# Kernel tuning notes

Hardware: AMD Instinct MI355X
Metric: run time of the kernel (lower is better)

Reference implementation:

```python
import jax, jax.numpy as jnp
import numpy as np

B, T, C = 2, 2048, 1024
NH, HD = 16, 64  # n_head, head_dim (qk == vo)


def setup_inputs() -> dict:
    key = jax.random.key(0)
    ks = jax.random.split(key, 5)
    scale = 1.0 / np.sqrt(C)
    return {
        "x": jax.random.normal(ks[0], (B, T, C), dtype=jnp.float32),
        "Wq": jax.random.normal(ks[1], (C, C), dtype=jnp.float32) * scale,
        "Wk": jax.random.normal(ks[2], (C, C), dtype=jnp.float32) * scale,
        "Wv": jax.random.normal(ks[3], (C, C), dtype=jnp.float32) * scale,
        "Wo": jax.random.normal(ks[4], (C, C), dtype=jnp.float32) * scale,
    }


def reference(x, Wq, Wk, Wv, Wo):
    # torch Linear: y = x @ W.T (weights stored [out, in])
    q = (x @ Wq.T).reshape(B, T, NH, HD).transpose(0, 2, 1, 3)  # [B,H,T,D]
    k = (x @ Wk.T).reshape(B, T, NH, HD).transpose(0, 2, 1, 3)
    v = (x @ Wv.T).reshape(B, T, NH, HD).transpose(0, 2, 1, 3)
    att = jnp.einsum("bhqd,bhkd->bhqk", q, k) * (1.0 / np.sqrt(HD))
    causal = jnp.tril(jnp.ones((T, T), dtype=bool))
    att = jnp.where(causal[None, None], att, -jnp.inf)
    att = jax.nn.softmax(att, axis=-1)
    y = jnp.einsum("bhqk,bhkd->bhqd", att, v)  # [B,H,T,D]
    y = y.transpose(0, 2, 1, 3).reshape(B, T, NH * HD)
    return y @ Wo.T  # dropout p=0 -> identity
```

## Files before the change

### kernel.cpp

```cpp
#include <hip/hip_runtime.h>
#include <hip/hip_bf16.h>
#include <cstdint>
#include <cstddef>
#include <cmath>

#define B_  2
#define T_  2048
#define C_  1024
#define NH_ 16
#define HD_ 64

typedef __bf16 bf16;
typedef bf16  bf16x8 __attribute__((ext_vector_type(8)));
typedef bf16  bf16x4 __attribute__((ext_vector_type(4)));
typedef float f32x4  __attribute__((ext_vector_type(4)));
typedef float f32x16 __attribute__((ext_vector_type(16)));

#define MFMA16(a, b, c) __builtin_amdgcn_mfma_f32_16x16x32_bf16((a), (b), (c), 0, 0, 0)
#define MFMA32(a, b, c) __builtin_amdgcn_mfma_f32_32x32x16_bf16((a), (b), (c), 0, 0, 0)

__device__ __forceinline__ void gld_lds16(const bf16* g, bf16* lds_base_uniform) {
    __builtin_amdgcn_global_load_lds(
        (const __attribute__((address_space(1))) uint32_t*)g,
        (__attribute__((address_space(3))) uint32_t*)lds_base_uniform,
        16, 0, 0);
}

__global__ __launch_bounds__(256) void cast_all(const float* __restrict__ x,
                                                const float* __restrict__ Wq,
                                                const float* __restrict__ Wk,
                                                const float* __restrict__ Wv,
                                                const float* __restrict__ Wo,
                                                bf16* __restrict__ xb,
                                                bf16* __restrict__ Wqk,
                                                bf16* __restrict__ Wvb,
                                                bf16* __restrict__ Wob) {
    const int bid = blockIdx.x;
    if (bid < 4096) {
        const int i = bid * 256 + threadIdx.x;
        float4 v = ((const float4*)x)[i];
        ((bf16x4*)xb)[i] = bf16x4{ (bf16)v.x, (bf16)v.y, (bf16)v.z, (bf16)v.w };
    } else {
        const float C1 = 0.1803368801111f;
        const int i = (bid - 4096) * 256 + threadIdx.x;
        const int nw4 = C_ * C_ / 4;
        float4 q = ((const float4*)Wq)[i];
        float4 k = ((const float4*)Wk)[i];
        float4 v = ((const float4*)Wv)[i];
        float4 o = ((const float4*)Wo)[i];
        ((bf16x4*)Wqk)[i]       = bf16x4{ (bf16)(q.x * C1), (bf16)(q.y * C1),
                                          (bf16)(q.z * C1), (bf16)(q.w * C1) };
        ((bf16x4*)Wqk)[nw4 + i] = bf16x4{ (bf16)k.x, (bf16)k.y, (bf16)k.z, (bf16)k.w };
        ((bf16x4*)Wvb)[i]       = bf16x4{ (bf16)v.x, (bf16)v.y, (bf16)v.z, (bf16)v.w };
        ((bf16x4*)Wob)[i]       = bf16x4{ (bf16)o.x, (bf16)o.y, (bf16)o.z, (bf16)o.w };
    }
}

__device__ __forceinline__ void gemm_tile(bf16* As, bf16* Bs,
                                          const bf16* __restrict__ A,
                                          const bf16* __restrict__ W,
                                          bf16* __restrict__ Y,
                                          int N, int K, int m0, int n0) {
    const int tid  = threadIdx.x;
    const int lane = tid & 63;
    const int w    = tid >> 6;
    const int ml   = lane & 15;
    const int quad = lane >> 4;
    const int wm   = (w >> 1) * 64;
    const int wn   = (w & 1) * 64;
    const int sr   = lane >> 2;
    const int sc   = lane & 3;

    f32x4 acc[4][4] = {};

    for (int k0 = 0; k0 < K; k0 += 32) {
        __syncthreads();
#pragma unroll
        for (int ei = 0; ei < 2; ++ei) {
            const int e = w * 2 + ei;
            gld_lds16(A + (size_t)(m0 + e * 16 + sr) * K + k0 + sc * 8, &As[e * 512]);
            gld_lds16(W + (size_t)(n0 + e * 16 + sr) * K + k0 + sc * 8, &Bs[e * 512]);
        }
        __builtin_amdgcn_s_waitcnt(0);
        __syncthreads();

        bf16x8 af[4], bfr[4];
#pragma unroll
        for (int t = 0; t < 4; ++t) {
            af[t]  = *(const bf16x8*)&As[(wm + t * 16 + ml) * 32 + quad * 8];
            bfr[t] = *(const bf16x8*)&Bs[(wn + t * 16 + ml) * 32 + quad * 8];
        }
#pragma unroll
        for (int mt = 0; mt < 4; ++mt)
#pragma unroll
            for (int nt = 0; nt < 4; ++nt)
                acc[mt][nt] = MFMA16(af[mt], bfr[nt], acc[mt][nt]);
    }

#pragma unroll
    for (int mt = 0; mt < 4; ++mt)
#pragma unroll
        for (int nt = 0; nt < 4; ++nt)
#pragma unroll
            for (int r = 0; r < 4; ++r) {
                const int row = m0 + wm + mt * 16 + quad * 4 + r;
                const int col = n0 + wn + nt * 16 + ml;
                Y[(size_t)row * N + col] = (bf16)acc[mt][nt][r];
            }
}

__global__ __launch_bounds__(256) void proj_fused(const bf16* __restrict__ xb,
                                                  const bf16* __restrict__ Wqk,
                                                  const bf16* __restrict__ Wvb,
                                                  bf16* __restrict__ QKb,
                                                  bf16* __restrict__ VtT) {
    __shared__ __align__(16) bf16 As[128 * 32];
    __shared__ __align__(16) bf16 Bs[128 * 32];
    const int bid = blockIdx.x;
    if (bid < 512) {
        gemm_tile(As, Bs, xb, Wqk, QKb, 2048, 1024, (bid >> 4) * 128, (bid & 15) * 128);
    } else {
        const int b2 = bid - 512;
        gemm_tile(As, Bs, Wvb, xb, VtT, 4096, 1024, (b2 >> 5) * 128, (b2 & 31) * 128);
    }
}

__global__ __launch_bounds__(256) void gemm_wo(const bf16* __restrict__ A,
                                               const bf16* __restrict__ W,
                                               float* __restrict__ Y) {
    __shared__ __align__(16) bf16 As[64 * 32];
    __shared__ __align__(16) bf16 Bs[128 * 32];
    const int tid  = threadIdx.x;
    const int lane = tid & 63;
    const int w    = tid >> 6;
    const int ml   = lane & 15;
    const int quad = lane >> 4;
    const int wm   = (w >> 1) * 32;
    const int wn   = (w & 1) * 64;
    const int m0   = blockIdx.y * 64;
    const int n0   = blockIdx.x * 128;
    const int sr   = lane >> 2;
    const int sc   = lane & 3;

    f32x4 acc[2][4] = {};

    for (int k0 = 0; k0 < 1024; k0 += 32) {
        __syncthreads();
        gld_lds16(A + (size_t)(m0 + w * 16 + sr) * 1024 + k0 + sc * 8, &As[w * 512]);
#pragma unroll
        for (int ei = 0; ei < 2; ++ei) {
            const int e = w * 2 + ei;
            gld_lds16(W + (size_t)(n0 + e * 16 + sr) * 1024 + k0 + sc * 8, &Bs[e * 512]);
        }
        __builtin_amdgcn_s_waitcnt(0);
        __syncthreads();

        bf16x8 af[2], bfr[4];
#pragma unroll
        for (int t = 0; t < 2; ++t)
            af[t] = *(const bf16x8*)&As[(wm + t * 16 + ml) * 32 + quad * 8];
#pragma unroll
        for (int t = 0; t < 4; ++t)
            bfr[t] = *(const bf16x8*)&Bs[(wn + t * 16 + ml) * 32 + quad * 8];
#pragma unroll
        for (int mt = 0; mt < 2; ++mt)
#pragma unroll
            for (int nt = 0; nt < 4; ++nt)
                acc[mt][nt] = MFMA16(af[mt], bfr[nt], acc[mt][nt]);
    }

#pragma unroll
    for (int mt = 0; mt < 2; ++mt)
#pragma unroll
        for (int nt = 0; nt < 4; ++nt)
#pragma unroll
            for (int r = 0; r < 4; ++r) {
                const int row = m0 + wm + mt * 16 + quad * 4 + r;
                const int col = n0 + wn + nt * 16 + ml;
                Y[(size_t)row * 1024 + col] = acc[mt][nt][r];
            }
}

__global__ __launch_bounds__(256, 3) void attn_mfma(const bf16* __restrict__ QKb,
                                                    const bf16* __restrict__ VtT,
                                                    bf16* __restrict__ Pbuf,
                                                    float* __restrict__ Lbuf) {
    const int bid = blockIdx.x;
    const int hb  = bid & 31;
    const int s   = 39 - (bid >> 5);
    int it, chunk;
    if (s < 4)       { it = s;                  chunk = 0; }
    else if (s < 12) { it = 4 + ((s - 4) >> 1); chunk = (s - 4) & 1; }
    else if (s < 24) { it = 8 + (s - 12) / 3;   chunk = (s - 12) % 3; }
    else             { it = 12 + ((s - 24) >> 2); chunk = (s - 24) & 3; }
    const int h = hb >> 1, b = hb & 1;

    const int tid  = threadIdx.x;
    const int lane = tid & 63;
    const int w    = tid >> 6;
    const int keyl = lane & 31;
    const int hi   = lane >> 5;

    __shared__ __align__(16) bf16 Ks[2][4096];
    __shared__ __align__(16) bf16 Vs[2][4096];
    __shared__ __align__(16) bf16 Ps[4][2048];

    const bf16* Qbase = QKb + (size_t)b * T_ * 2048 + (size_t)h * HD_;
    const bf16* Kbase = Qbase + 1024;
    const bf16* Vbase = VtT + (size_t)h * HD_ * 4096 + (size_t)b * T_;

    const int qrow = it * 128 + w * 32 + keyl;
    bf16x8 qf[4];
#pragma unroll
    for (int dc = 0; dc < 4; ++dc)
        qf[dc] = *(const bf16x8*)(Qbase + (size_t)qrow * 2048 + dc * 16 + hi * 8);

    f32x16 o_acc[2] = {};
    f32x16 l_acc = {};
    bf16x8 onesf;
#pragma unroll
    for (int j = 0; j < 8; ++j) onesf[j] = (bf16)1.0f;

    bf16* ps = &Ps[w][0];
    uint16_t* ps16 = (uint16_t*)ps;

    const int ktbase  = chunk * 8;
    const int nrounds = min(8, 2 * it + 2 - ktbase);

    auto stageKV = [&](int ktg, int buf) {
        const int k0 = ktg * 64;
#pragma unroll
        for (int ei = 0; ei < 2; ++ei) {
            const int e  = w * 2 + ei;
            const int rr = e * 8 + (lane >> 3);
            const int g  = (lane & 7) ^ (lane >> 3);
            gld_lds16(Kbase + (size_t)(k0 + rr) * 2048 + g * 8, &Ks[buf][e * 512]);
            gld_lds16(Vbase + (size_t)rr * 4096 + k0 + g * 8, &Vs[buf][e * 512]);
        }
    };

    auto phase1 = [&](int cur, int ktg) {
        const int k0 = ktg * 64;
        const bool domask = (k0 + 63) > (it * 128 + w * 32);
#pragma unroll
        for (int kh = 0; kh < 2; ++kh) {
            f32x16 sacc = {};
#pragma unroll
            for (int dc = 0; dc < 4; ++dc) {
                bf16x8 kf = *(const bf16x8*)&Ks[cur][(kh * 32 + keyl) * 64 +
                                                     ((((dc << 1) | hi)) ^ (keyl & 7)) * 8];
                sacc = MFMA32(qf[dc], kf, sacc);
            }
            const int kg = k0 + kh * 32 + keyl;
#pragma unroll
            for (int r = 0; r < 16; ++r) {
                float arg = sacc[r];
                const int qloc = (r & 3) + 8 * (r >> 2) + 4 * hi;
                if (domask) {
                    const int qg = it * 128 + w * 32 + qloc;
                    if (kg > qg) arg = -1e30f;
                }
                const float p = __builtin_amdgcn_exp2f(arg);
                ps16[qloc * 64 + (((kh * 4 + (keyl >> 3)) ^ (qloc & 7)) << 3) + (keyl & 7)] =
                    (uint16_t)(__builtin_bit_cast(uint32_t, p) >> 16);
            }
        }
    };

    auto phase2 = [&](int cur) {
        bf16x8 pa[4];
#pragma unroll
        for (int kc = 0; kc < 4; ++kc) {
            pa[kc] = *(const bf16x8*)&ps[keyl * 64 + (((kc << 1) | hi) ^ (keyl & 7)) * 8];
            l_acc = MFMA32(pa[kc], onesf, l_acc);
        }
#pragma unroll
        for (int dh = 0; dh < 2; ++dh)
#pragma unroll
            for (int kc = 0; kc < 4; ++kc) {
                bf16x8 vf = *(const bf16x8*)&Vs[cur][(dh * 32 + keyl) * 64 +
                                                     (((kc << 1) | hi) ^ (keyl & 7)) * 8];
                o_acc[dh] = MFMA32(pa[kc], vf, o_acc[dh]);
            }
    };

    stageKV(ktbase, 0);
    asm volatile("s_waitcnt vmcnt(0)" ::: "memory");
    asm volatile("s_barrier" ::: "memory");

    for (int j = 0; j < nrounds; ++j) {
        const int cur = j & 1;
        const int ktg = ktbase + j;
        if (j + 1 < nrounds) stageKV(ktg + 1, cur ^ 1);
        phase1(cur, ktg);
        phase2(cur);
        if (j + 1 < nrounds) {
            asm volatile("s_waitcnt vmcnt(0)" ::: "memory");
            asm volatile("s_barrier" ::: "memory");
        }
    }

    const int slotIdx = hb * 40 + s;
    bf16* pb = Pbuf + (size_t)slotIdx * 8192;
#pragma unroll
    for (int dh = 0; dh < 2; ++dh)
#pragma unroll
        for (int r = 0; r < 16; ++r) {
            const int qloc = w * 32 + (r & 3) + 8 * (r >> 2) + 4 * hi;
            pb[qloc * 64 + dh * 32 + keyl] = (bf16)o_acc[dh][r];
        }
    if (keyl == 0) {
#pragma unroll
        for (int r = 0; r < 16; ++r) {
            const int qloc = w * 32 + (r & 3) + 8 * (r >> 2) + 4 * hi;
            Lbuf[slotIdx * 128 + qloc] = l_acc[r];
        }
    }
}

__global__ __launch_bounds__(256) void attn_merge(const bf16* __restrict__ Pbuf,
                                                  const float* __restrict__ Lbuf,
                                                  bf16* __restrict__ Ab) {
    const int gid = blockIdx.x;
    const int it  = gid >> 5;
    const int hb  = gid & 31;
    const int h = hb >> 1, b = hb & 1;
    int s0;
    if (it < 4)       s0 = it;
    else if (it < 8)  s0 = 4 + (it - 4) * 2;
    else if (it < 12) s0 = 12 + (it - 8) * 3;
    else              s0 = 24 + (it - 12) * 4;
    const int nch = (2 * it + 9) >> 3;

    const int tid = threadIdx.x;
    const int row = tid >> 1;
    const int cg  = (tid & 1) * 32;

    float acc[32] = {};
    float lsum = 0.f;
    for (int c = 0; c < nch; ++c) {
        const int slot = hb * 40 + s0 + c;
        lsum += Lbuf[slot * 128 + row];
        const bf16* pb = Pbuf + (size_t)slot * 8192 + row * 64 + cg;
#pragma unroll
        for (int g = 0; g < 4; ++g) {
            bf16x8 v = *(const bf16x8*)(pb + g * 8);
#pragma unroll
            for (int j = 0; j < 8; ++j) acc[g * 8 + j] += (float)v[j];
        }
    }
    const float rcl = 1.0f / lsum;
    bf16* dst = Ab + (size_t)(b * T_ + it * 128 + row) * 1024 + h * 64 + cg;
#pragma unroll
    for (int g = 0; g < 4; ++g) {
        bf16x8 o;
#pragma unroll
        for (int j = 0; j < 8; ++j) o[j] = (bf16)(acc[g * 8 + j] * rcl);
        *(bf16x8*)(dst + g * 8) = o;
    }
}

extern "C" void kernel_launch(void* const* d_in, const int* in_sizes, int n_in,
                              void* d_out, int out_size, void* d_ws, size_t ws_size,
                              hipStream_t stream) {
    const float* x  = (const float*)d_in[0];
    const float* Wq = (const float*)d_in[1];
    const float* Wk = (const float*)d_in[2];
    const float* Wv = (const float*)d_in[3];
    const float* Wo = (const float*)d_in[4];
    float* out = (float*)d_out;

    const size_t n_x = (size_t)B_ * T_ * C_;
    const size_t n_w = (size_t)C_ * C_;

    bf16* xb   = (bf16*)d_ws;
    bf16* Wqk  = xb + n_x;
    bf16* Wvb  = Wqk + 2 * n_w;
    bf16* Wob  = Wvb + n_w;
    bf16* QKb  = Wob + n_w;
    bf16* VtT  = QKb + 2 * n_x;
    bf16* Ab   = VtT + n_x;
    bf16* Pbuf = Ab + n_x;
    float* Lbuf = (float*)(Pbuf + (size_t)1280 * 8192);

    cast_all<<<5120, 256, 0, stream>>>(x, Wq, Wk, Wv, Wo, xb, Wqk, Wvb, Wob);

    proj_fused<<<768, 256, 0, stream>>>(xb, Wqk, Wvb, QKb, VtT);

    attn_mfma<<<1280, 256, 0, stream>>>(QKb, VtT, Pbuf, Lbuf);
    attn_merge<<<512, 256, 0, stream>>>(Pbuf, Lbuf, Ab);

    gemm_wo<<<dim3(1024 / 128, 4096 / 64), 256, 0, stream>>>(Ab, Wob, out);
}
```

Before: 181.9 us.

## Keep attention probabilities in registers via transposed S MFMA and permlane swap

Computes S transposed (K as the A operand) so each lane holds one query's scores, then packs the exp'd probabilities to bf16 and uses v_permlane32_swap to form the PV MFMA operand directly in registers. This removes the per-wave LDS P buffer round trip and the ones-vector MFMA used for row sums, which are now accumulated as a scalar per lane and combined with a cross-half shuffle. Freeing the P LDS lets launch bounds rise from 3 to 5 blocks per CU. The risk is higher register pressure under the tighter occupancy bound, which could cause spills.

```diff
diff --git a/kernel.cpp b/kernel.cpp
--- a/kernel.cpp
+++ b/kernel.cpp
@@ -181,7 +181,7 @@
             }
 }
 
-__global__ __launch_bounds__(256, 3) void attn_mfma(const bf16* __restrict__ QKb,
+__global__ __launch_bounds__(256, 5) void attn_mfma(const bf16* __restrict__ QKb,
                                                     const bf16* __restrict__ VtT,
                                                     bf16* __restrict__ Pbuf,
                                                     float* __restrict__ Lbuf) {
@@ -203,7 +203,6 @@
 
     __shared__ __align__(16) bf16 Ks[2][4096];
     __shared__ __align__(16) bf16 Vs[2][4096];
-    __shared__ __align__(16) bf16 Ps[4][2048];
 
     const bf16* Qbase = QKb + (size_t)b * T_ * 2048 + (size_t)h * HD_;
     const bf16* Kbase = Qbase + 1024;
@@ -216,13 +215,7 @@
         qf[dc] = *(const bf16x8*)(Qbase + (size_t)qrow * 2048 + dc * 16 + hi * 8);
 
     f32x16 o_acc[2] = {};
-    f32x16 l_acc = {};
-    bf16x8 onesf;
-#pragma unroll
-    for (int j = 0; j < 8; ++j) onesf[j] = (bf16)1.0f;
-
-    bf16* ps = &Ps[w][0];
-    uint16_t* ps16 = (uint16_t*)ps;
+    float l_run = 0.f;
 
     const int ktbase  = chunk * 8;
     const int nrounds = min(8, 2 * it + 2 - ktbase);
@@ -239,49 +232,50 @@
         }
     };
 
-    auto phase1 = [&](int cur, int ktg) {
+    auto round = [&](int cur, int ktg) {
         const int k0 = ktg * 64;
         const bool domask = (k0 + 63) > (it * 128 + w * 32);
+        const int qg = it * 128 + w * 32 + keyl;
 #pragma unroll
         for (int kh = 0; kh < 2; ++kh) {
             f32x16 sacc = {};
 #pragma unroll
             for (int dc = 0; dc < 4; ++dc) {
                 bf16x8 kf = *(const bf16x8*)&Ks[cur][(kh * 32 + keyl) * 64 +
-                                                     ((((dc << 1) | hi)) ^ (keyl & 7)) * 8];
-                sacc = MFMA32(qf[dc], kf, sacc);
+                                                     (((dc << 1) | hi) ^ (keyl & 7)) * 8];
+                sacc = MFMA32(kf, qf[dc], sacc);
             }
-            const int kg = k0 + kh * 32 + keyl;
-#pragma unroll
-            for (int r = 0; r < 16; ++r) {
-                float arg = sacc[r];
-                const int qloc = (r & 3) + 8 * (r >> 2) + 4 * hi;
-                if (domask) {
-                    const int qg = it * 128 + w * 32 + qloc;
-                    if (kg > qg) arg = -1e30f;
+#pragma unroll
+            for (int c = 0; c < 2; ++c) {
+                float p[8];
+#pragma unroll
+                for (int r8 = 0; r8 < 8; ++r8) {
+                    float arg = sacc[8 * c + r8];
+                    if (domask) {
+                        const int kg = k0 + kh * 32 + 16 * c + 8 * (r8 >> 2) + 4 * hi + (r8 & 3);
+                        if (kg > qg) arg = -1e30f;
+                    }
+                    p[r8] = __builtin_amdgcn_exp2f(arg);
                 }
-                const float p = __builtin_amdgcn_exp2f(arg);
-                ps16[qloc * 64 + (((kh * 4 + (keyl >> 3)) ^ (qloc & 7)) << 3) + (keyl & 7)] =
-                    (uint16_t)(__builtin_bit_cast(uint32_t, p) >> 16);
+                l_run += ((p[0] + p[1]) + (p[2] + p[3])) + ((p[4] + p[5]) + (p[6] + p[7]));
+                uint32_t a0, a1, b0, b1;
+                asm("v_cvt_pk_bf16_f32 %0, %1, %2" : "=v"(a0) : "v"(p[0]), "v"(p[1]));
+                asm("v_cvt_pk_bf16_f32 %0, %1, %2" : "=v"(a1) : "v"(p[2]), "v"(p[3]));
+                asm("v_cvt_pk_bf16_f32 %0, %1, %2" : "=v"(b0) : "v"(p[4]), "v"(p[5]));
+                asm("v_cvt_pk_bf16_f32 %0, %1, %2" : "=v"(b1) : "v"(p[6]), "v"(p[7]));
+                asm("v_permlane32_swap_b32 %0, %1" : "+v"(a0), "+v"(b0));
+                asm("v_permlane32_swap_b32 %0, %1" : "+v"(a1), "+v"(b1));
+                union { uint32_t d[4]; bf16x8 v; } pa;
+                pa.d[0] = a0; pa.d[1] = a1; pa.d[2] = b0; pa.d[3] = b1;
+                const int kc = 2 * kh + c;
+#pragma unroll
+                for (int dh = 0; dh < 2; ++dh) {
+                    bf16x8 vf = *(const bf16x8*)&Vs[cur][(dh * 32 + keyl) * 64 +
+                                                         (((kc << 1) | hi) ^ (keyl & 7)) * 8];
+                    o_acc[dh] = MFMA32(pa.v, vf, o_acc[dh]);
+                }
             }
         }
-    };
-
-    auto phase2 = [&](int cur) {
-        bf16x8 pa[4];
-#pragma unroll
-        for (int kc = 0; kc < 4; ++kc) {
-            pa[kc] = *(const bf16x8*)&ps[keyl * 64 + (((kc << 1) | hi) ^ (keyl & 7)) * 8];
-            l_acc = MFMA32(pa[kc], onesf, l_acc);
-        }
-#pragma unroll
-        for (int dh = 0; dh < 2; ++dh)
-#pragma unroll
-            for (int kc = 0; kc < 4; ++kc) {
-                bf16x8 vf = *(const bf16x8*)&Vs[cur][(dh * 32 + keyl) * 64 +
-                                                     (((kc << 1) | hi) ^ (keyl & 7)) * 8];
-                o_acc[dh] = MFMA32(pa[kc], vf, o_acc[dh]);
-            }
     };
 
     stageKV(ktbase, 0);
@@ -292,8 +286,7 @@
         const int cur = j & 1;
         const int ktg = ktbase + j;
         if (j + 1 < nrounds) stageKV(ktg + 1, cur ^ 1);
-        phase1(cur, ktg);
-        phase2(cur);
+        round(cur, ktg);
         if (j + 1 < nrounds) {
             asm volatile("s_waitcnt vmcnt(0)" ::: "memory");
             asm volatile("s_barrier" ::: "memory");
@@ -309,13 +302,9 @@
             const int qloc = w * 32 + (r & 3) + 8 * (r >> 2) + 4 * hi;
             pb[qloc * 64 + dh * 32 + keyl] = (bf16)o_acc[dh][r];
         }
-    if (keyl == 0) {
-#pragma unroll
-        for (int r = 0; r < 16; ++r) {
-            const int qloc = w * 32 + (r & 3) + 8 * (r >> 2) + 4 * hi;
-            Lbuf[slotIdx * 128 + qloc] = l_acc[r];
-        }
-    }
+    const float l_tot = l_run + __shfl_xor(l_run, 32);
+    if (hi == 0)
+        Lbuf[slotIdx * 128 + w * 32 + keyl] = l_tot;
 }
 
 __global__ __launch_bounds__(256) void attn_merge(const bf16* __restrict__ Pbuf,
```

New measurement: 199.0 us. 1.09x slower.
